# Optimization experiments

Measured on AMD Instinct MI355X. Metric: run time of the kernel, lower is better.

Reference implementation:

```python
import jax, jax.numpy as jnp
import numpy as np

VOC, D, CPR, RELS = 2048, 128, 128, 7
B, DEPTH = 512, 4  # complete binary trees: 2**DEPTH leaves per tree


def setup_inputs() -> dict:
    key = jax.random.key(0)
    ks = jax.random.split(key, 13)
    s = lambda k, shape, fan: jax.random.normal(k, shape, jnp.float32) / np.sqrt(fan)
    return {
        "leaf_ids": jax.random.randint(ks[0], (B, 2, 2 ** DEPTH), 0, VOC),
        "Wv": s(ks[1], (D, VOC), VOC), "bv": jnp.zeros((D,), jnp.float32),
        "Wcps": s(ks[2], (D, 2 * D), 2 * D), "bcps": jnp.zeros((D,), jnp.float32),
        "Wcpst": s(ks[3], (D, D * D), D * D), "bcpst": jnp.zeros((D,), jnp.float32),
        "Wcpr": s(ks[4], (CPR, 2 * D), 2 * D), "bcpr": jnp.zeros((CPR,), jnp.float32),
        "Wcprt": s(ks[5], (CPR, D * D), D * D), "bcprt": jnp.zeros((CPR,), jnp.float32),
        "Wsm": s(ks[6], (RELS, CPR), CPR), "bsm": jnp.zeros((RELS,), jnp.float32),
    }


def reference(leaf_ids, Wv, bv, Wcps, bcps, Wcpst, bcpst, Wcpr, bcpr, Wcprt, bcprt, Wsm, bsm):
    d = Wv.shape[0]
    # leaf embedding: voc(one_hot(idx)) == Wv[:, idx] + bv  -> [B, 2, L, d]
    h = jnp.take(Wv.T, leaf_ids, axis=0) + bv
    # batched level-by-level tree composition (complete binary trees)
    while h.shape[2] > 1:
        l, r = h[:, :, 0::2, :], h[:, :, 1::2, :]
        lin = jnp.concatenate([l, r], axis=-1) @ Wcps.T + bcps
        kron = (l[..., :, None] * r[..., None, :]).reshape(l.shape[:-1] + (d * d,))
        h = jnp.tanh(lin + kron @ Wcpst.T + bcpst)
    lc, rc = h[:, 0, 0, :], h[:, 1, 0, :]  # [B, d] each
    cpr = jnp.concatenate([lc, rc], axis=-1) @ Wcpr.T + bcpr
    kron = (lc[:, :, None] * rc[:, None, :]).reshape(lc.shape[0], d * d)
    act = jax.nn.leaky_relu(cpr + kron @ Wcprt.T + bcprt, 0.01)
    logits = act @ Wsm.T + bsm
    return jax.nn.log_softmax(logits, axis=-1)  # [B, RELS]
```

## Files before the change

### kernel.cpp

```cpp
#include <hip/hip_runtime.h>
#include <hip/hip_bf16.h>
#include <hip/hip_fp16.h>

#define DD    128
#define VOCAB 2048
#define NRELS 7
#define NWF   (130 * 16384)

typedef _Float16 f16;
typedef __attribute__((ext_vector_type(8))) _Float16 f16x8;
typedef __attribute__((ext_vector_type(4))) float    f32x4;

__device__ __forceinline__ float lde(const void* p, size_t i, int bf) {
    if (bf) return (float)((const __hip_bfloat16*)p)[i];
    return ((const float*)p)[i];
}

__device__ __forceinline__ int detect_bf(const unsigned short* wv) {
    int sane = 0;
    #pragma unroll
    for (int i = 0; i < 64; ++i) {
        unsigned e = (wv[i] >> 7) & 0xFFu;
        sane += (e >= 90u && e <= 160u) ? 1 : 0;
    }
    return sane == 64;
}

template<int N>
__device__ __forceinline__ void wait_vmcnt() {
    asm volatile("s_waitcnt vmcnt(%0)" :: "n"(N) : "memory");
}

__global__ void prep_all(const void* Wv, const void* bv,
                         const void* Wcps, const void* bcps,
                         const void* Wcpst, const void* bcpst,
                         const void* Wcpr, const void* bcpr,
                         const void* Wcprt, const void* bcprt,
                         const void* Wsm, const void* bsm,
                         f16* __restrict__ WvT, f16* __restrict__ Wext, f16* __restrict__ Wfin,
                         float* __restrict__ bias_lvl, float* __restrict__ bias_fin,
                         float* __restrict__ Wsm_f, float* __restrict__ bsm_f)
{
    const int bf = detect_bf((const unsigned short*)Wv);
    const int b = blockIdx.x;
    const int tid = threadIdx.x;

    if (b < 64) {
        __shared__ float tile[64][65];
        int vt = b >> 1, dt = b & 1;
        int tx = tid & 63, ty = tid >> 6;
        for (int yy = ty; yy < 64; yy += 4)
            tile[yy][tx] = lde(Wv, (size_t)(dt * 64 + yy) * VOCAB + vt * 64 + tx, bf);
        __syncthreads();
        for (int yy = ty; yy < 64; yy += 4) {
            int v = vt * 64 + yy, d = dt * 64 + tx;
            __builtin_nontemporal_store((f16)(tile[tx][yy] + lde(bv, d, bf)),
                                        &WvT[(size_t)v * DD + d]);
        }
        return;
    }
    if (b >= 2144) {
        if (tid < 128)      bias_lvl[tid] = lde(bcps, tid, bf) + lde(bcpst, tid, bf);
        else if (tid < 256) bias_fin[tid - 128] = lde(bcpr, tid - 128, bf) + lde(bcprt, tid - 128, bf);
        for (int o = tid; o < NRELS * DD; o += 256) Wsm_f[o] = lde(Wsm, o, bf);
        if (tid < NRELS) bsm_f[tid] = lde(bsm, tid, bf);
        return;
    }
    const int bb    = b - 64;
    const int which = bb / 1040;
    const int rem   = bb - which * 1040;
    const int i     = rem >> 3;
    const int n8    = rem & 7;
    const void* Wt = which ? (const void*)Wcprt : (const void*)Wcpst;
    const void* Ws = which ? (const void*)Wcpr  : (const void*)Wcps;
    f16* dst = which ? Wfin : Wext;

    __shared__ float tile[16 * 129];
    #pragma unroll
    for (int it = 0; it < 8; ++it) {
        int idx = it * 256 + tid;
        int rr = idx >> 7, c = idx & 127;
        float v = (i < 128) ? lde(Wt, (size_t)(n8 * 16 + rr) * 16384 + (size_t)i * 128 + c, bf)
                            : lde(Ws, (size_t)(n8 * 16 + rr) * 256 + (size_t)(i - 128) * 128 + c, bf);
        tile[rr * 129 + c] = v;
    }
    __syncthreads();
    f16* out = dst + (size_t)(i * 8 + n8) * 2048;
    #pragma unroll
    for (int it = 0; it < 8; ++it) {
        int o = it * 256 + tid;
        int t = o >> 9, ln = (o >> 3) & 63, e = o & 7;
        __builtin_nontemporal_store((f16)tile[(ln & 15) * 129 + t * 32 + ((ln >> 4) << 3) + e],
                                    &out[o]);
    }
}

template<int BI>
__launch_bounds__(256, 2)
__global__ void gemm_kernel(const f16* __restrict__ hin, const int* __restrict__ ids,
                            const f16* __restrict__ Wf,
                            f16* __restrict__ part, int Mrows, int S)
{
    __shared__ f16 Wb[4][8192];

    const int tid  = threadIdx.x;
    const int lane = tid & 63;
    const int wv   = tid >> 6;
    const int b    = blockIdx.x;
    const int nh   = (b >> 2) & 1;
    const int r    = ((b >> 3) << 2) | (b & 3);
    const int mb   = r / S;
    const int s    = r - mb * S;
    const int m0   = mb * 256;
    const int i0   = s * BI;
    const bool tail = (s == 1 || s == 2);
    const int itail = (s == 1) ? 128 : 129;

    const int mrow = lane & 15;
    const int q    = lane >> 4;
    const int wm   = wv * 64;

    f16x8 rf[4][4];
    int rowL[4];
    #pragma unroll
    for (int mt = 0; mt < 4; ++mt) {
        int p = m0 + wm + mt * 16 + mrow;
        int row = ids ? ids[2 * p + 1] : 2 * p + 1;
        rowL[mt] = ids ? ids[2 * p] : 2 * p;
        #pragma unroll
        for (int t = 0; t < 4; ++t)
            rf[mt][t] = *(const f16x8*)&hin[(size_t)row * DD + t * 32 + q * 8];
    }

    f16 lw[4][BI];
    #pragma unroll
    for (int mt = 0; mt < 4; ++mt) {
        const f16* src = &hin[(size_t)rowL[mt] * DD + i0];
        if constexpr (BI == 16) { *(f16x8*)&lw[mt][0] = *(const f16x8*)src;
                                  *(f16x8*)&lw[mt][8] = *(const f16x8*)(src + 8); }
        else if constexpr (BI == 8) { *(f16x8*)&lw[mt][0] = *(const f16x8*)src; }
        else if constexpr (BI == 4) { *(unsigned long long*)&lw[mt][0] = *(const unsigned long long*)src; }
        else if constexpr (BI == 2) { *(unsigned int*)&lw[mt][0] = *(const unsigned int*)src; }
        else { lw[mt][0] = src[0]; }
    }

    auto stage = [&](int i, int slot) {
        const f16* g = Wf + (size_t)i * 16384 + nh * 8192;
        #pragma unroll
        for (int k = 0; k < 4; ++k) {
            int j = k * 4 + wv;
            const f16* gg = g + (size_t)(j * 64 + lane) * 8;
            f16* l = &Wb[slot][(size_t)(j * 64) * 8];
            __builtin_amdgcn_global_load_lds(
                (const __attribute__((address_space(1))) unsigned int*)gg,
                (__attribute__((address_space(3))) unsigned int*)l, 16, 0, 0);
        }
    };

    stage(i0, 0);
    stage(i0 + 1, 1);
    if constexpr (BI >= 3) {
        stage(i0 + 2, 2);
        wait_vmcnt<8>();
    } else {
        if (tail) stage(itail, 2);
        wait_vmcnt<4>();
    }
    __builtin_amdgcn_s_barrier();

    f32x4 acc[4][4] = {};

#define TSTEP(T, SLOT, KRON, LBV)                                                       \
    {                                                                                   \
        f16x8 wc[4];                                                                    \
        _Pragma("unroll")                                                               \
        for (int nt = 0; nt < 4; ++nt)                                                  \
            wc[nt] = *(const f16x8*)&Wb[SLOT][nt * 2048 + (T) * 512 + lane * 8];        \
        _Pragma("unroll")                                                               \
        for (int mt = 0; mt < 4; ++mt) {                                                \
            f16x8 a = (KRON) ? (LBV[mt] * rf[mt][T]) : rf[mt][T];                       \
            _Pragma("unroll")                                                           \
            for (int nt = 0; nt < 4; ++nt)                                              \
                acc[mt][nt] = __builtin_amdgcn_mfma_f32_16x16x32_f16(a, wc[nt], acc[mt][nt], 0, 0, 0); \
        }                                                                               \
    }

    #pragma unroll
    for (int ii = 0; ii < BI; ++ii) {
        if constexpr (BI >= 3) {
            if (ii + 3 < BI)                stage(i0 + ii + 3, (ii + 3) & 3);
            else if (ii + 3 == BI && tail)  stage(itail, BI & 3);
        }
        if (ii <= BI - 4)       wait_vmcnt<8>();
        else if (ii == BI - 3)  wait_vmcnt<4>();
        else                    wait_vmcnt<0>();
        f16x8 lb[4];
        #pragma unroll
        for (int mt = 0; mt < 4; ++mt) {
            f16 v = lw[mt][ii];
            #pragma unroll
            for (int e = 0; e < 8; ++e) lb[mt][e] = v;
        }
        __builtin_amdgcn_s_setprio(1);
        TSTEP(0, ii & 3, true, lb); TSTEP(1, ii & 3, true, lb);
        TSTEP(2, ii & 3, true, lb); TSTEP(3, ii & 3, true, lb);
        __builtin_amdgcn_s_setprio(0);
        if (ii + 1 < BI || tail) __builtin_amdgcn_s_barrier();
    }

    if (tail) {
        constexpr int slot = BI & 3;
        if (s == 1) {
            #pragma unroll
            for (int mt = 0; mt < 4; ++mt)
                #pragma unroll
                for (int t = 0; t < 4; ++t)
                    rf[mt][t] = *(const f16x8*)&hin[(size_t)rowL[mt] * DD + t * 32 + q * 8];
        }
        f16x8 dummy[4];
        __builtin_amdgcn_s_setprio(1);
        TSTEP(0, slot, false, dummy); TSTEP(1, slot, false, dummy);
        TSTEP(2, slot, false, dummy); TSTEP(3, slot, false, dummy);
        __builtin_amdgcn_s_setprio(0);
    }
#undef TSTEP

    f16* pb = part + ((size_t)s * Mrows + m0) * DD + nh * 64;
    #pragma unroll
    for (int mt = 0; mt < 4; ++mt)
        #pragma unroll
        for (int nt = 0; nt < 4; ++nt) {
            int colg = nt * 16 + mrow;
            #pragma unroll
            for (int rr = 0; rr < 4; ++rr) {
                int rowl = wm + mt * 16 + q * 4 + rr;
                pb[(size_t)rowl * DD + colg] = (f16)acc[mt][nt][rr];
            }
        }
}

__global__ void epi_level(const f16* __restrict__ part, const float* __restrict__ bias,
                          f16* __restrict__ hout, int Mrows, int S)
{
    int idx = (blockIdx.x * 256 + threadIdx.x) * 8;
    size_t stride = (size_t)Mrows * DD;
    float sum[8] = {};
    for (int s2 = 0; s2 < S; ++s2) {
        f16x8 v = *(const f16x8*)&part[(size_t)s2 * stride + idx];
        #pragma unroll
        for (int e = 0; e < 8; ++e) sum[e] += (float)v[e];
    }
    int n = idx & 127;
    f16x8 o;
    #pragma unroll
    for (int e = 0; e < 8; ++e) o[e] = (f16)tanhf(sum[e] + bias[n + e]);
    *(f16x8*)&hout[idx] = o;
}

__global__ void fin_epi(const f16* __restrict__ part, const float* __restrict__ bias,
                        const float* __restrict__ Wsm_f, const float* __restrict__ bsm_f,
                        const unsigned short* __restrict__ wv_raw, void* __restrict__ outp, int S)
{
    int lane = threadIdx.x & 63;
    int wv = threadIdx.x >> 6;
    int p = blockIdx.x * 4 + wv;
    size_t stride = (size_t)512 * DD;
    const f16* base = part + (size_t)p * DD;
    float a0 = 0.f, a1 = 0.f;
    for (int s2 = 0; s2 < S; ++s2) {
        a0 += (float)base[(size_t)s2 * stride + lane];
        a1 += (float)base[(size_t)s2 * stride + 64 + lane];
    }
    a0 += bias[lane];      a1 += bias[64 + lane];
    a0 = (a0 > 0.f) ? a0 : 0.01f * a0;
    a1 = (a1 > 0.f) ? a1 : 0.01f * a1;
    float lg[NRELS];
    #pragma unroll
    for (int r = 0; r < NRELS; ++r) {
        float pr = a0 * Wsm_f[r * DD + lane] + a1 * Wsm_f[r * DD + 64 + lane];
        #pragma unroll
        for (int d = 1; d < 64; d <<= 1) pr += __shfl_xor(pr, d, 64);
        lg[r] = pr + bsm_f[r];
    }
    float mx = lg[0];
    #pragma unroll
    for (int r = 1; r < NRELS; ++r) mx = fmaxf(mx, lg[r]);
    float se = 0.f;
    #pragma unroll
    for (int r = 0; r < NRELS; ++r) se += expf(lg[r] - mx);
    float lse = logf(se) + mx;
    if (lane < NRELS) {
        float v = lg[lane] - lse;
        if (detect_bf(wv_raw)) ((__hip_bfloat16*)outp)[p * NRELS + lane] = __float2bfloat16(v);
        else                   ((float*)outp)[p * NRELS + lane] = v;
    }
}

extern "C" void kernel_launch(void* const* d_in, const int* in_sizes, int n_in,
                              void* d_out, int out_size, void* d_ws, size_t ws_size,
                              hipStream_t stream)
{
    const int* ids = (const int*)d_in[0];

    char* ws = (char*)d_ws;
    f16*   part     = (f16*)ws;
    f16*   h1       = (f16*)(ws + ((size_t)32 << 20));
    f16*   h2       = (f16*)(ws + ((size_t)34 << 20));
    f16*   h3       = (f16*)(ws + ((size_t)35 << 20));
    f16*   h4       = (f16*)(ws + ((size_t)35 << 20) + (512 << 10));
    f16*   WvT      = (f16*)(ws + ((size_t)36 << 20));
    f16*   Wext     = (f16*)(ws + ((size_t)36 << 20) + (512 << 10));
    f16*   Wfin     = Wext + (size_t)NWF;
    float* bias_lvl = (float*)(Wfin + (size_t)NWF);
    float* bias_fin = bias_lvl + 128;
    float* Wsm_f    = bias_fin + 128;
    float* bsm_f    = Wsm_f + NRELS * DD;

    if (ws_size < ((size_t)48 << 20)) return;

    prep_all<<<2145, 256, 0, stream>>>(d_in[1], d_in[2], d_in[3], d_in[4], d_in[5], d_in[6],
                                       d_in[7], d_in[8], d_in[9], d_in[10], d_in[11], d_in[12],
                                       WvT, Wext, Wfin, bias_lvl, bias_fin, Wsm_f, bsm_f);

    gemm_kernel<8><<<1024, 256, 0, stream>>>(WvT, ids, Wext, part, 8192, 16);
    epi_level<<<512, 256, 0, stream>>>(part, bias_lvl, h1, 8192, 16);
    gemm_kernel<8><<<512, 256, 0, stream>>>(h1, nullptr, Wext, part, 4096, 16);
    epi_level<<<256, 256, 0, stream>>>(part, bias_lvl, h2, 4096, 16);
    gemm_kernel<4><<<512, 256, 0, stream>>>(h2, nullptr, Wext, part, 2048, 32);
    epi_level<<<128, 256, 0, stream>>>(part, bias_lvl, h3, 2048, 32);
    gemm_kernel<4><<<256, 256, 0, stream>>>(h3, nullptr, Wext, part, 1024, 32);
    epi_level<<<64, 256, 0, stream>>>(part, bias_lvl, h4, 1024, 32);
    gemm_kernel<2><<<256, 256, 0, stream>>>(h4, nullptr, Wfin, part, 512, 64);
    fin_epi<<<128, 256, 0, stream>>>(part, bias_fin, Wsm_f, bsm_f,
                                     (const unsigned short*)d_in[1], d_out, 64);
}
```

Baseline: 259.6 us.

## Fuse split-K reduction and tanh epilogue into GEMM via last-block atomic counter

Removes the separate epi_level launches. Each GEMM block now bumps a per-output-tile atomic counter after writing its split-K partial, and the last-arriving block sums all partials, adds the bias, applies tanh and writes the next level's activations. Block indexing is remapped so split index s is the high bits, which changes block-to-tile scheduling. This saves four kernel launches and their gaps, at the cost of a serialized reduction tail in one block per tile and reliance on threadfence/atomic ordering for correctness.

New measurement: 504.7 us. 1.94x slower.

```diff
diff --git a/kernel.cpp b/kernel.cpp
--- a/kernel.cpp
+++ b/kernel.cpp
@@ -39,7 +39,8 @@
                          const void* Wsm, const void* bsm,
                          f16* __restrict__ WvT, f16* __restrict__ Wext, f16* __restrict__ Wfin,
                          float* __restrict__ bias_lvl, float* __restrict__ bias_fin,
-                         float* __restrict__ Wsm_f, float* __restrict__ bsm_f)
+                         float* __restrict__ Wsm_f, float* __restrict__ bsm_f,
+                         unsigned* __restrict__ cnt)
 {
     const int bf = detect_bf((const unsigned short*)Wv);
     const int b = blockIdx.x;
@@ -60,8 +61,12 @@
         return;
     }
     if (b >= 2144) {
-        if (tid < 128)      bias_lvl[tid] = lde(bcps, tid, bf) + lde(bcpst, tid, bf);
-        else if (tid < 256) bias_fin[tid - 128] = lde(bcpr, tid - 128, bf) + lde(bcprt, tid - 128, bf);
+        if (tid < 128) {
+            bias_lvl[tid] = lde(bcps, tid, bf) + lde(bcpst, tid, bf);
+            cnt[tid] = 0u;
+        } else if (tid < 256) {
+            bias_fin[tid - 128] = lde(bcpr, tid - 128, bf) + lde(bcprt, tid - 128, bf);
+        }
         for (int o = tid; o < NRELS * DD; o += 256) Wsm_f[o] = lde(Wsm, o, bf);
         if (tid < NRELS) bsm_f[tid] = lde(bsm, tid, bf);
         return;
@@ -95,11 +100,13 @@
     }
 }
 
-template<int BI>
+template<int BI, bool FUSE>
 __launch_bounds__(256, 2)
 __global__ void gemm_kernel(const f16* __restrict__ hin, const int* __restrict__ ids,
                             const f16* __restrict__ Wf,
-                            f16* __restrict__ part, int Mrows, int S)
+                            f16* __restrict__ part, int Mrows, int S,
+                            unsigned* __restrict__ cnt, const float* __restrict__ bias,
+                            f16* __restrict__ hout)
 {
     __shared__ f16 Wb[4][8192];
 
@@ -107,10 +114,12 @@
     const int lane = tid & 63;
     const int wv   = tid >> 6;
     const int b    = blockIdx.x;
-    const int nh   = (b >> 2) & 1;
-    const int r    = ((b >> 3) << 2) | (b & 3);
-    const int mb   = r / S;
-    const int s    = r - mb * S;
+    const int ngroups = Mrows >> 7;
+    const int lg   = 31 - __builtin_clz(ngroups);
+    const int s    = b >> lg;
+    const int gid  = b & (ngroups - 1);
+    const int mb   = gid >> 1;
+    const int nh   = gid & 1;
     const int m0   = mb * 256;
     const int i0   = s * BI;
     const bool tail = (s == 1 || s == 2);
@@ -136,12 +145,10 @@
     #pragma unroll
     for (int mt = 0; mt < 4; ++mt) {
         const f16* src = &hin[(size_t)rowL[mt] * DD + i0];
-        if constexpr (BI == 16) { *(f16x8*)&lw[mt][0] = *(const f16x8*)src;
-                                  *(f16x8*)&lw[mt][8] = *(const f16x8*)(src + 8); }
-        else if constexpr (BI == 8) { *(f16x8*)&lw[mt][0] = *(const f16x8*)src; }
+        if constexpr (BI == 8)      { *(f16x8*)&lw[mt][0] = *(const f16x8*)src; }
         else if constexpr (BI == 4) { *(unsigned long long*)&lw[mt][0] = *(const unsigned long long*)src; }
         else if constexpr (BI == 2) { *(unsigned int*)&lw[mt][0] = *(const unsigned int*)src; }
-        else { lw[mt][0] = src[0]; }
+        else                        { lw[mt][0] = src[0]; }
     }
 
     auto stage = [&](int i, int slot) {
@@ -209,7 +216,7 @@
     }
 
     if (tail) {
-        constexpr int slot = BI & 3;
+        constexpr int slot = (BI >= 3) ? (BI & 3) : 2;
         if (s == 1) {
             #pragma unroll
             for (int mt = 0; mt < 4; ++mt)
@@ -237,24 +244,39 @@
                 pb[(size_t)rowl * DD + colg] = (f16)acc[mt][nt][rr];
             }
         }
-}
-
-__global__ void epi_level(const f16* __restrict__ part, const float* __restrict__ bias,
-                          f16* __restrict__ hout, int Mrows, int S)
-{
-    int idx = (blockIdx.x * 256 + threadIdx.x) * 8;
-    size_t stride = (size_t)Mrows * DD;
-    float sum[8] = {};
-    for (int s2 = 0; s2 < S; ++s2) {
-        f16x8 v = *(const f16x8*)&part[(size_t)s2 * stride + idx];
-        #pragma unroll
-        for (int e = 0; e < 8; ++e) sum[e] += (float)v[e];
-    }
-    int n = idx & 127;
-    f16x8 o;
-    #pragma unroll
-    for (int e = 0; e < 8; ++e) o[e] = (f16)tanhf(sum[e] + bias[n + e]);
-    *(f16x8*)&hout[idx] = o;
+
+    if constexpr (FUSE) {
+        __syncthreads();
+        volatile int* flagp = (volatile int*)&Wb[0][0];
+        if (tid == 0) {
+            __threadfence();
+            unsigned old = atomicAdd(&cnt[gid], 1u);
+            *flagp = (old == (unsigned)(S - 1)) ? 1 : 0;
+        }
+        __syncthreads();
+        if (*flagp == 0) return;
+        __threadfence();
+        const size_t stride = (size_t)Mrows * DD;
+        const f16* pr = part + (size_t)m0 * DD + nh * 64;
+        #pragma unroll
+        for (int it = 0; it < 8; ++it) {
+            int vi   = it * 256 + tid;
+            int rowl = vi >> 3, cv = vi & 7;
+            size_t off = (size_t)rowl * DD + cv * 8;
+            float sum[8] = {};
+            for (int s2 = 0; s2 < S; ++s2) {
+                f16x8 v = *(const f16x8*)&pr[(size_t)s2 * stride + off];
+                #pragma unroll
+                for (int e = 0; e < 8; ++e) sum[e] += (float)v[e];
+            }
+            int ncol = nh * 64 + cv * 8;
+            f16x8 o;
+            #pragma unroll
+            for (int e = 0; e < 8; ++e) o[e] = (f16)tanhf(sum[e] + bias[ncol + e]);
+            *(f16x8*)&hout[(size_t)(m0 + rowl) * DD + ncol] = o;
+        }
+        if (tid == 0) atomicExch(&cnt[gid], 0u);
+    }
 }
 
 __global__ void fin_epi(const f16* __restrict__ part, const float* __restrict__ bias,
@@ -315,22 +337,24 @@
     float* bias_fin = bias_lvl + 128;
     float* Wsm_f    = bias_fin + 128;
     float* bsm_f    = Wsm_f + NRELS * DD;
+    unsigned* cnt   = (unsigned*)(bsm_f + NRELS);
 
     if (ws_size < ((size_t)48 << 20)) return;
 
     prep_all<<<2145, 256, 0, stream>>>(d_in[1], d_in[2], d_in[3], d_in[4], d_in[5], d_in[6],
                                        d_in[7], d_in[8], d_in[9], d_in[10], d_in[11], d_in[12],
-                                       WvT, Wext, Wfin, bias_lvl, bias_fin, Wsm_f, bsm_f);
-
-    gemm_kernel<8><<<1024, 256, 0, stream>>>(WvT, ids, Wext, part, 8192, 16);
-    epi_level<<<512, 256, 0, stream>>>(part, bias_lvl, h1, 8192, 16);
-    gemm_kernel<8><<<512, 256, 0, stream>>>(h1, nullptr, Wext, part, 4096, 16);
-    epi_level<<<256, 256, 0, stream>>>(part, bias_lvl, h2, 4096, 16);
-    gemm_kernel<4><<<512, 256, 0, stream>>>(h2, nullptr, Wext, part, 2048, 32);
-    epi_level<<<128, 256, 0, stream>>>(part, bias_lvl, h3, 2048, 32);
-    gemm_kernel<4><<<256, 256, 0, stream>>>(h3, nullptr, Wext, part, 1024, 32);
-    epi_level<<<64, 256, 0, stream>>>(part, bias_lvl, h4, 1024, 32);
-    gemm_kernel<2><<<256, 256, 0, stream>>>(h4, nullptr, Wfin, part, 512, 64);
+                                       WvT, Wext, Wfin, bias_lvl, bias_fin, Wsm_f, bsm_f, cnt);
+
+    gemm_kernel<8, true ><<<1024, 256, 0, stream>>>(WvT, ids, Wext, part, 8192, 16,
+                                                    cnt +   0, bias_lvl, h1);
+    gemm_kernel<8, true ><<<512, 256, 0, stream>>>(h1, nullptr, Wext, part, 4096, 16,
+                                                   cnt +  64, bias_lvl, h2);
+    gemm_kernel<4, true ><<<512, 256, 0, stream>>>(h2, nullptr, Wext, part, 2048, 32,
+                                                   cnt +  96, bias_lvl, h3);
+    gemm_kernel<4, true ><<<256, 256, 0, stream>>>(h3, nullptr, Wext, part, 1024, 32,
+                                                   cnt + 112, bias_lvl, h4);
+    gemm_kernel<2, false><<<256, 256, 0, stream>>>(h4, nullptr, Wfin, part, 512, 64,
+                                                   nullptr, nullptr, nullptr);
     fin_epi<<<128, 256, 0, stream>>>(part, bias_fin, Wsm_f, bsm_f,
                                      (const unsigned short*)d_in[1], d_out, 64);
 }
```

## Add wide-N GEMM variant covering all 128 output columns for first level

Applied to the files above, without the earlier changes.

Adds a gemm_wide kernel where each block computes the full 128-column output instead of splitting N in halves. This halves the block count for the first tree level and avoids loading the gathered A rows twice. It also switches to double-buffered 32KB weight stages with a full vmcnt wait each iteration. The cost is a larger accumulator footprint (4x8 tiles) that may raise register pressure and reduce occupancy, and less overlap between loads and compute.

New measurement: 309.6 us. 1.19x slower.

```diff
diff --git a/kernel.cpp b/kernel.cpp
--- a/kernel.cpp
+++ b/kernel.cpp
@@ -93,6 +93,137 @@
         __builtin_nontemporal_store((f16)tile[(ln & 15) * 129 + t * 32 + ((ln >> 4) << 3) + e],
                                     &out[o]);
     }
+}
+
+template<int BI>
+__launch_bounds__(256, 2)
+__global__ void gemm_wide(const f16* __restrict__ hin, const int* __restrict__ ids,
+                          const f16* __restrict__ Wf,
+                          f16* __restrict__ part, int Mrows, int S)
+{
+    __shared__ f16 Wb[2][16384];
+
+    const int tid  = threadIdx.x;
+    const int lane = tid & 63;
+    const int wv   = tid >> 6;
+    const int b    = blockIdx.x;
+    const int s    = b & (S - 1);
+    const int mb   = b >> 4;
+    const int m0   = mb * 256;
+    const int i0   = s * BI;
+    const bool tail = (s == 1 || s == 2);
+    const int itail = (s == 1) ? 128 : 129;
+
+    const int mrow = lane & 15;
+    const int q    = lane >> 4;
+    const int wm   = wv * 64;
+
+    f16x8 rf[4][4];
+    int rowL[4];
+    #pragma unroll
+    for (int mt = 0; mt < 4; ++mt) {
+        int p = m0 + wm + mt * 16 + mrow;
+        int row = ids ? ids[2 * p + 1] : 2 * p + 1;
+        rowL[mt] = ids ? ids[2 * p] : 2 * p;
+        #pragma unroll
+        for (int t = 0; t < 4; ++t)
+            rf[mt][t] = *(const f16x8*)&hin[(size_t)row * DD + t * 32 + q * 8];
+    }
+
+    f16 lw[4][BI];
+    #pragma unroll
+    for (int mt = 0; mt < 4; ++mt) {
+        const f16* src = &hin[(size_t)rowL[mt] * DD + i0];
+        if constexpr (BI == 8)      { *(f16x8*)&lw[mt][0] = *(const f16x8*)src; }
+        else if constexpr (BI == 4) { *(unsigned long long*)&lw[mt][0] = *(const unsigned long long*)src; }
+        else if constexpr (BI == 2) { *(unsigned int*)&lw[mt][0] = *(const unsigned int*)src; }
+        else                        { lw[mt][0] = src[0]; }
+    }
+
+    auto stage = [&](int i, int slot) {
+        const f16* g = Wf + (size_t)i * 16384;
+        #pragma unroll
+        for (int k = 0; k < 8; ++k) {
+            int j = k * 4 + wv;
+            const f16* gg = g + (size_t)(j * 64 + lane) * 8;
+            f16* l = &Wb[slot][(size_t)(j * 64) * 8];
+            __builtin_amdgcn_global_load_lds(
+                (const __attribute__((address_space(1))) unsigned int*)gg,
+                (__attribute__((address_space(3))) unsigned int*)l, 16, 0, 0);
+        }
+    };
+
+    stage(i0, 0);
+    wait_vmcnt<0>();
+    __builtin_amdgcn_s_barrier();
+
+    f32x4 acc[4][8] = {};
+
+#define TSTEP(T4, SLOT, KRON, LBV)                                                      \
+    {                                                                                   \
+        f16x8 a[4];                                                                     \
+        _Pragma("unroll")                                                               \
+        for (int mt = 0; mt < 4; ++mt)                                                  \
+            a[mt] = (KRON) ? (LBV[mt] * rf[mt][T4]) : rf[mt][T4];                       \
+        _Pragma("unroll")                                                               \
+        for (int nt = 0; nt < 8; ++nt) {                                                \
+            f16x8 wc = *(const f16x8*)&Wb[SLOT][nt * 2048 + (T4) * 512 + lane * 8];     \
+            _Pragma("unroll")                                                           \
+            for (int mt = 0; mt < 4; ++mt)                                              \
+                acc[mt][nt] = __builtin_amdgcn_mfma_f32_16x16x32_f16(a[mt], wc, acc[mt][nt], 0, 0, 0); \
+        }                                                                               \
+    }
+
+    #pragma unroll
+    for (int ii = 0; ii < BI; ++ii) {
+        if (ii + 1 < BI)          stage(i0 + ii + 1, (ii + 1) & 1);
+        else if (tail)            stage(itail, BI & 1);
+        f16x8 lb[4];
+        #pragma unroll
+        for (int mt = 0; mt < 4; ++mt) {
+            f16 v = lw[mt][ii];
+            #pragma unroll
+            for (int e = 0; e < 8; ++e) lb[mt][e] = v;
+        }
+        __builtin_amdgcn_s_setprio(1);
+        TSTEP(0, ii & 1, true, lb); TSTEP(1, ii & 1, true, lb);
+        TSTEP(2, ii & 1, true, lb); TSTEP(3, ii & 1, true, lb);
+        __builtin_amdgcn_s_setprio(0);
+        if (ii + 1 < BI || tail) {
+            wait_vmcnt<0>();
+            __builtin_amdgcn_s_barrier();
+        }
+    }
+
+    if (tail) {
+        constexpr int slot = BI & 1;
+        if (s == 1) {
+            #pragma unroll
+            for (int mt = 0; mt < 4; ++mt)
+                #pragma unroll
+                for (int t = 0; t < 4; ++t)
+                    rf[mt][t] = *(const f16x8*)&hin[(size_t)rowL[mt] * DD + t * 32 + q * 8];
+        }
+        f16x8 dummy[4];
+        __builtin_amdgcn_s_setprio(1);
+        TSTEP(0, slot, false, dummy); TSTEP(1, slot, false, dummy);
+        TSTEP(2, slot, false, dummy); TSTEP(3, slot, false, dummy);
+        __builtin_amdgcn_s_setprio(0);
+    }
+#undef TSTEP
+
+    f16* pb = part + ((size_t)s * Mrows + m0) * DD;
+    #pragma unroll
+    for (int mt = 0; mt < 4; ++mt)
+        #pragma unroll
+        for (int nt = 0; nt < 8; ++nt) {
+            int colg = nt * 16 + mrow;
+            #pragma unroll
+            for (int rr = 0; rr < 4; ++rr) {
+                int rowl = wm + mt * 16 + q * 4 + rr;
+                pb[(size_t)rowl * DD + colg] = (f16)acc[mt][nt][rr];
+            }
+        }
 }
 
 template<int BI>
@@ -136,12 +267,10 @@
     #pragma unroll
     for (int mt = 0; mt < 4; ++mt) {
         const f16* src = &hin[(size_t)rowL[mt] * DD + i0];
-        if constexpr (BI == 16) { *(f16x8*)&lw[mt][0] = *(const f16x8*)src;
-                                  *(f16x8*)&lw[mt][8] = *(const f16x8*)(src + 8); }
-        else if constexpr (BI == 8) { *(f16x8*)&lw[mt][0] = *(const f16x8*)src; }
+        if constexpr (BI == 8)      { *(f16x8*)&lw[mt][0] = *(const f16x8*)src; }
         else if constexpr (BI == 4) { *(unsigned long long*)&lw[mt][0] = *(const unsigned long long*)src; }
         else if constexpr (BI == 2) { *(unsigned int*)&lw[mt][0] = *(const unsigned int*)src; }
-        else { lw[mt][0] = src[0]; }
+        else                        { lw[mt][0] = src[0]; }
     }
 
     auto stage = [&](int i, int slot) {
@@ -209,7 +338,7 @@
     }
 
     if (tail) {
-        constexpr int slot = BI & 3;
+        constexpr int slot = (BI >= 3) ? (BI & 3) : 2;
         if (s == 1) {
             #pragma unroll
             for (int mt = 0; mt < 4; ++mt)
@@ -322,7 +451,7 @@
                                        d_in[7], d_in[8], d_in[9], d_in[10], d_in[11], d_in[12],
                                        WvT, Wext, Wfin, bias_lvl, bias_fin, Wsm_f, bsm_f);
 
-    gemm_kernel<8><<<1024, 256, 0, stream>>>(WvT, ids, Wext, part, 8192, 16);
+    gemm_wide<8><<<512, 256, 0, stream>>>(WvT, ids, Wext, part, 8192, 16);
     epi_level<<<512, 256, 0, stream>>>(part, bias_lvl, h1, 8192, 16);
     gemm_kernel<8><<<512, 256, 0, stream>>>(h1, nullptr, Wext, part, 4096, 16);
     epi_level<<<256, 256, 0, stream>>>(part, bias_lvl, h2, 4096, 16);
```
